# Kernel tuning notes

Measured on AMD Instinct MI355X. Metric: run time of the kernel, lower is better.

## Reference

```python
import jax, jax.numpy as jnp
import numpy as np

B, S, DIM = 2, 2048, 2048
NUM_HEADS, HEAD_DIM, KV_PER = 16, 128, 1
NUM_KV = NUM_HEADS * KV_PER  # = 16; code requires KV_PER == 1 for shape consistency
QKV_OUT = (NUM_HEADS + 2 * NUM_KV) * HEAD_DIM


def setup_inputs() -> dict:
    key = jax.random.key(0)
    k1, k2, k3 = jax.random.split(key, 3)
    x = jax.random.normal(k1, (B, S, DIM), dtype=jnp.float32)
    w_qkv = jax.random.normal(k2, (DIM, QKV_OUT), dtype=jnp.float32) * (DIM ** -0.5)
    w_out = jax.random.normal(k3, (NUM_HEADS * HEAD_DIM, DIM), dtype=jnp.float32) * ((NUM_HEADS * HEAD_DIM) ** -0.5)
    return {"x": x, "w_qkv": w_qkv, "w_out": w_out}


def reference(x, w_qkv, w_out):
    b, s, _ = x.shape
    # QKV projection, then split heads: [b, s, nq + 2*nkv, d]
    qkv = (x @ w_qkv).reshape(b, s, NUM_HEADS + 2 * NUM_KV, HEAD_DIM)
    q = qkv[:, :, :NUM_HEADS]                          # [b, s, nq, d]
    k = qkv[:, :, NUM_HEADS:NUM_HEADS + NUM_KV]        # [b, s, nkv, d]
    v = qkv[:, :, NUM_HEADS + NUM_KV:]                 # [b, s, nkv, d]
    # query -> [b, nkv, per, s, d] (per == KV_PER == 1)
    q = q.reshape(b, s, NUM_KV, KV_PER, HEAD_DIM).transpose(0, 2, 3, 1, 4)
    k = k.transpose(0, 2, 1, 3)                        # [b, nkv, s, d]
    v = v.transpose(0, 2, 1, 3)                        # [b, nkv, s, d]
    scale = 1.0 / (HEAD_DIM ** 0.5)
    # logits: [b, nkv, per, s_q, s_k]
    logits = jnp.einsum('bkpsd,bktd->bkpst', q, k) * scale
    attn = jax.nn.softmax(logits.astype(jnp.float32), axis=-1)
    # combined: [b, nkv, per, s, d] -> [b, s, nkv, per, d] -> [b, s, dim]
    combined = jnp.einsum('bkpst,bktd->bkpsd', attn, v.astype(jnp.float32)).astype(v.dtype)
    combined = combined.transpose(0, 3, 1, 2, 4).reshape(b, s, NUM_KV * KV_PER * HEAD_DIM)
    return combined @ w_out
```

## Files before the change

kernel.cpp:

```cpp
#include <hip/hip_runtime.h>
#include <cstdint>

typedef __bf16 bf16x8 __attribute__((ext_vector_type(8)));
typedef float f32x4 __attribute__((ext_vector_type(4)));
typedef unsigned short u16x8 __attribute__((ext_vector_type(8)));

#define NH 16
#define HD 128
#define SEQ 2048
#define DIM 2048
#define QKVO 6144

__device__ __forceinline__ unsigned short f32_bf16(float f) {
  uint32_t u = __builtin_bit_cast(uint32_t, f);
  u += 0x7fffu + ((u >> 16) & 1u);
  return (unsigned short)(u >> 16);
}

__device__ __forceinline__ uint32_t cvt_pk_bf16(float a, float b) {
  uint32_t r;
  asm("v_cvt_pk_bf16_f32 %0, %1, %2" : "=v"(r) : "v"(a), "v"(b));
  return r;
}

__device__ __forceinline__ void gl2lds16(const void* g, void* l) {
  __builtin_amdgcn_global_load_lds(
      (const __attribute__((address_space(1))) uint32_t*)g,
      (__attribute__((address_space(3))) uint32_t*)l,
      16, 0, 0);
}

__global__ __launch_bounds__(256) void cvt_f32_bf16(
    const float* __restrict__ in, unsigned short* __restrict__ out) {
  long i = ((long)blockIdx.x * 256 + threadIdx.x) * 8;
  f32x4 a = *(const f32x4*)(in + i);
  f32x4 b = *(const f32x4*)(in + i + 4);
  u16x8 r;
#pragma unroll
  for (int j = 0; j < 4; j++) { r[j] = f32_bf16(a[j]); r[4 + j] = f32_bf16(b[j]); }
  *(u16x8*)(out + i) = r;
}

__global__ __launch_bounds__(256) void transpose_f32_bf16(
    const float* __restrict__ in, unsigned short* __restrict__ out,
    int R, int C) {
  __shared__ unsigned short tile[64][65];
  const int t = threadIdx.x, tx = t & 63, ty = t >> 6;
  const long r0 = (long)blockIdx.y * 64, c0 = (long)blockIdx.x * 64;
  for (int i = 0; i < 16; i++) {
    int row = ty + i * 4;
    tile[row][tx] = f32_bf16(in[(r0 + row) * C + c0 + tx]);
  }
  __syncthreads();
  for (int i = 0; i < 16; i++) {
    int row = ty + i * 4;
    out[(c0 + row) * R + r0 + tx] = tile[tx][row];
  }
}

__global__ __launch_bounds__(256) void transpose_v(
    const unsigned short* __restrict__ qkv, unsigned short* __restrict__ vT) {
  __shared__ unsigned short tile[64][65];
  const int t = threadIdx.x, tx = t & 63, ty = t >> 6;
  const int bh = blockIdx.z, b = bh >> 4, h = bh & 15;
  const long t0 = (long)blockIdx.x * 64;
  const int d0 = blockIdx.y * 64;
  const unsigned short* src = qkv + (long)b * SEQ * QKVO + 2 * NH * HD + h * HD;
  for (int i = 0; i < 16; i++) {
    int row = ty + i * 4;
    tile[row][tx] = src[(t0 + row) * QKVO + d0 + tx];
  }
  __syncthreads();
  unsigned short* dst = vT + ((long)bh * HD + d0) * SEQ + t0;
  for (int i = 0; i < 16; i++) {
    int row = ty + i * 4;
    dst[(long)row * SEQ + tx] = tile[tx][row];
  }
}

template <typename OutT>
__global__ __launch_bounds__(256) void gemm_bt(
    const unsigned short* __restrict__ A, int lda,
    const unsigned short* __restrict__ BT, int ldb,
    OutT* __restrict__ C, int ldc, int K) {
  __shared__ __align__(16) unsigned short As[128 * 32];
  __shared__ __align__(16) unsigned short Bs[128 * 32];
  const int t = threadIdx.x;
  const int lane = t & 63, w = t >> 6;
  const int quad = lane >> 4, l16 = lane & 15;
  const int wm = (w & 1) * 64, wn = (w >> 1) * 64;
  const long m0 = (long)blockIdx.y * 128, n0 = (long)blockIdx.x * 128;

  f32x4 acc[4][4] = {};
  const int rowA = t >> 2, kslot = (t & 3) * 8;
  const unsigned short* Ag = A + (m0 + rowA) * (long)lda + kslot;
  const unsigned short* Bg = BT + (n0 + rowA) * (long)ldb + kslot;
  unsigned short* AsBase = &As[w * 512];
  unsigned short* BsBase = &Bs[w * 512];

  for (int k0 = 0; k0 < K; k0 += 32) {
    __syncthreads();
    gl2lds16(Ag + k0, AsBase);
    gl2lds16(Ag + 64 * (long)lda + k0, AsBase + 2048);
    gl2lds16(Bg + k0, BsBase);
    gl2lds16(Bg + 64 * (long)ldb + k0, BsBase + 2048);
    __syncthreads();

    bf16x8 af[4], bf[4];
#pragma unroll
    for (int mt = 0; mt < 4; mt++)
      af[mt] = *(const bf16x8*)&As[(wm + mt * 16 + l16) * 32 + quad * 8];
#pragma unroll
    for (int nt = 0; nt < 4; nt++)
      bf[nt] = *(const bf16x8*)&Bs[(wn + nt * 16 + l16) * 32 + quad * 8];
#pragma unroll
    for (int mt = 0; mt < 4; mt++)
#pragma unroll
      for (int nt = 0; nt < 4; nt++)
        acc[mt][nt] = __builtin_amdgcn_mfma_f32_16x16x32_bf16(
            af[mt], bf[nt], acc[mt][nt], 0, 0, 0);
  }

#pragma unroll
  for (int mt = 0; mt < 4; mt++) {
    long row = m0 + wm + mt * 16 + quad * 4;
#pragma unroll
    for (int r = 0; r < 4; r++) {
      OutT* crow = C + (row + r) * (long)ldc + n0 + wn + l16;
#pragma unroll
      for (int nt = 0; nt < 4; nt++) {
        float v = acc[mt][nt][r];
        if constexpr (sizeof(OutT) == 2) crow[nt * 16] = f32_bf16(v);
        else                             crow[nt * 16] = v;
      }
    }
  }
}

#define KSTR 136
#define VSTR 72
__global__ __launch_bounds__(256, 2) void attn_kernel(
    unsigned short* qkv, const unsigned short* __restrict__ vT) {
  __shared__ __align__(16) unsigned short Ks[64 * KSTR];
  __shared__ __align__(16) unsigned short Vs[128 * VSTR];
  __shared__ __align__(16) unsigned short Ps[4][32 * VSTR];

  const int t = threadIdx.x, lane = t & 63, w = t >> 6;
  const int quad = lane >> 4, l16 = lane & 15;
  const int q0 = blockIdx.x * 128, h = blockIdx.y, b = blockIdx.z;
  const long row0 = (long)b * SEQ;

  bf16x8 qf[2][4];
#pragma unroll
  for (int mt = 0; mt < 2; mt++) {
    const unsigned short* Qp =
        qkv + (row0 + q0 + w * 32 + mt * 16 + l16) * (long)QKVO + h * HD + quad * 8;
#pragma unroll
    for (int c = 0; c < 4; c++) qf[mt][c] = *(const bf16x8*)(Qp + c * 32);
  }

  float m_l[2], l_l[2];
  f32x4 o[2][8] = {};
  m_l[0] = m_l[1] = -1e30f;
  l_l[0] = l_l[1] = 0.f;
  const float c2 = 0.08838834764831845f * 1.4426950408889634f;
  const float thr = 8.0f / c2;

  const unsigned short* Kg = qkv + row0 * QKVO + NH * HD + h * HD;
  const unsigned short* Vg = vT + ((long)(b * NH + h)) * HD * SEQ;

  bf16x8 kr[4], vr[4];
#pragma unroll
  for (int i = 0; i < 4; i++) {
    int s = i * 256 + t;
    kr[i] = *(const bf16x8*)(Kg + (long)(s >> 4) * QKVO + (s & 15) * 8);
  }
#pragma unroll
  for (int i = 0; i < 4; i++) {
    int s = i * 256 + t;
    vr[i] = *(const bf16x8*)(Vg + (long)(s >> 3) * SEQ + (s & 7) * 8);
  }

  for (int kc = 0; kc < SEQ; kc += 64) {
    __syncthreads();
#pragma unroll
    for (int i = 0; i < 4; i++) {
      int s = i * 256 + t;
      *(bf16x8*)&Ks[(s >> 4) * KSTR + (s & 15) * 8] = kr[i];
    }
#pragma unroll
    for (int i = 0; i < 4; i++) {
      int s = i * 256 + t;
      *(bf16x8*)&Vs[(s >> 3) * VSTR + (s & 7) * 8] = vr[i];
    }
    __syncthreads();

    if (kc + 64 < SEQ) {
#pragma unroll
      for (int i = 0; i < 4; i++) {
        int s = i * 256 + t;
        kr[i] = *(const bf16x8*)(Kg + (long)(kc + 64 + (s >> 4)) * QKVO + (s & 15) * 8);
      }
#pragma unroll
      for (int i = 0; i < 4; i++) {
        int s = i * 256 + t;
        vr[i] = *(const bf16x8*)(Vg + (long)(s >> 3) * SEQ + kc + 64 + (s & 7) * 8);
      }
    }

    f32x4 st[2][4];
#pragma unroll
    for (int kt = 0; kt < 4; kt++) {
      f32x4 a0 = {}, a1 = {};
#pragma unroll
      for (int c = 0; c < 4; c++) {
        bf16x8 kf = *(const bf16x8*)&Ks[(kt * 16 + l16) * KSTR + c * 32 + quad * 8];
        a0 = __builtin_amdgcn_mfma_f32_16x16x32_bf16(kf, qf[0][c], a0, 0, 0, 0);
        a1 = __builtin_amdgcn_mfma_f32_16x16x32_bf16(kf, qf[1][c], a1, 0, 0, 0);
      }
      st[0][kt] = a0; st[1][kt] = a1;
    }

#pragma unroll
    for (int mt = 0; mt < 2; mt++) {
      float mx0 = fmaxf(fmaxf(st[mt][0][0], st[mt][0][1]),
                        fmaxf(st[mt][0][2], st[mt][0][3]));
      float mx1 = fmaxf(fmaxf(st[mt][1][0], st[mt][1][1]),
                        fmaxf(st[mt][1][2], st[mt][1][3]));
      float mx2 = fmaxf(fmaxf(st[mt][2][0], st[mt][2][1]),
                        fmaxf(st[mt][2][2], st[mt][2][3]));
      float mx3 = fmaxf(fmaxf(st[mt][3][0], st[mt][3][1]),
                        fmaxf(st[mt][3][2], st[mt][3][3]));
      float mx = fmaxf(fmaxf(mx0, mx1), fmaxf(mx2, mx3));
      mx = fmaxf(mx, __shfl_xor(mx, 16, 64));
      mx = fmaxf(mx, __shfl_xor(mx, 32, 64));

      if (__any(mx > m_l[mt] + thr)) {
        float mn = fmaxf(m_l[mt], mx);
        float alpha = exp2f(c2 * (m_l[mt] - mn));
        m_l[mt] = mn;
        l_l[mt] *= alpha;
        float a_o[4];
#pragma unroll
        for (int r = 0; r < 4; r++) a_o[r] = __shfl(alpha, (quad << 2) | r, 16);
#pragma unroll
        for (int dt = 0; dt < 8; dt++)
#pragma unroll
          for (int r = 0; r < 4; r++) o[mt][dt][r] *= a_o[r];
      }

      float cm = c2 * m_l[mt];
      float sum = 0.f;
      uint32_t pk0[4], pk1[4];
#pragma unroll
      for (int kt = 0; kt < 4; kt++) {
        float p0 = exp2f(fmaf(st[mt][kt][0], c2, -cm));
        float p1 = exp2f(fmaf(st[mt][kt][1], c2, -cm));
        float p2 = exp2f(fmaf(st[mt][kt][2], c2, -cm));
        float p3 = exp2f(fmaf(st[mt][kt][3], c2, -cm));
        sum += (p0 + p1) + (p2 + p3);
        pk0[kt] = cvt_pk_bf16(p0, p1);
        pk1[kt] = cvt_pk_bf16(p2, p3);
      }
      sum += __shfl_xor(sum, 16, 64);
      sum += __shfl_xor(sum, 32, 64);
      l_l[mt] += sum;

#pragma unroll
      for (int kt = 0; kt < 4; kt++) {
        uint2 w2; w2.x = pk0[kt]; w2.y = pk1[kt];
        *(uint2*)&Ps[w][(mt * 16 + l16) * VSTR + kt * 16 + quad * 4] = w2;
      }
    }
    asm volatile("s_waitcnt lgkmcnt(0)" ::: "memory");

#pragma unroll
    for (int cc = 0; cc < 2; cc++) {
      bf16x8 pf0 = *(const bf16x8*)&Ps[w][(l16) * VSTR + cc * 32 + quad * 8];
      bf16x8 pf1 = *(const bf16x8*)&Ps[w][(16 + l16) * VSTR + cc * 32 + quad * 8];
#pragma unroll
      for (int dt = 0; dt < 8; dt++) {
        bf16x8 vf = *(const bf16x8*)&Vs[(dt * 16 + l16) * VSTR + cc * 32 + quad * 8];
        o[0][dt] = __builtin_amdgcn_mfma_f32_16x16x32_bf16(pf0, vf, o[0][dt], 0, 0, 0);
        o[1][dt] = __builtin_amdgcn_mfma_f32_16x16x32_bf16(pf1, vf, o[1][dt], 0, 0, 0);
      }
    }
  }

  float inv_o[2][4];
#pragma unroll
  for (int mt = 0; mt < 2; mt++) {
    float linv = 1.f / l_l[mt];
#pragma unroll
    for (int r = 0; r < 4; r++) inv_o[mt][r] = __shfl(linv, (quad << 2) | r, 16);
  }
#pragma unroll
  for (int mt = 0; mt < 2; mt++) {
    long orow = row0 + q0 + w * 32 + mt * 16 + quad * 4;
    unsigned short* Op = qkv + orow * (long)QKVO + h * HD + l16;
#pragma unroll
    for (int r = 0; r < 4; r++) {
#pragma unroll
      for (int dt = 0; dt < 8; dt++)
        Op[(long)r * QKVO + dt * 16] = f32_bf16(o[mt][dt][r] * inv_o[mt][r]);
    }
  }
}

extern "C" void kernel_launch(void* const* d_in, const int* in_sizes, int n_in,
                              void* d_out, int out_size, void* d_ws, size_t ws_size,
                              hipStream_t stream) {
  const float* x     = (const float*)d_in[0];
  const float* w_qkv = (const float*)d_in[1];
  const float* w_out = (const float*)d_in[2];
  float* out = (float*)d_out;

  char* ws = (char*)d_ws;
  unsigned short* qkv   = (unsigned short*)ws;
  unsigned short* xbf   = (unsigned short*)(ws + 50331648);
  unsigned short* wqkvT = (unsigned short*)(ws + 67108864);
  unsigned short* vTbuf = (unsigned short*)(ws + 67108864);
  unsigned short* woutT = (unsigned short*)(ws + 83886080);

  dim3 blk(256);
  cvt_f32_bf16<<<4096, blk, 0, stream>>>(x, xbf);
  transpose_f32_bf16<<<dim3(QKVO / 64, DIM / 64), blk, 0, stream>>>(w_qkv, wqkvT, DIM, QKVO);
  gemm_bt<unsigned short><<<dim3(QKVO / 128, 4096 / 128), blk, 0, stream>>>(
      xbf, DIM, wqkvT, DIM, qkv, QKVO, DIM);
  transpose_v<<<dim3(SEQ / 64, HD / 64, 2 * NH), blk, 0, stream>>>(qkv, vTbuf);
  transpose_f32_bf16<<<dim3(DIM / 64, DIM / 64), blk, 0, stream>>>(w_out, woutT, DIM, DIM);
  attn_kernel<<<dim3(SEQ / 128, NH, 2), blk, 0, stream>>>(qkv, vTbuf);
  gemm_bt<float><<<dim3(DIM / 128, 4096 / 128), blk, 0, stream>>>(
      qkv, QKVO, woutT, DIM, out, DIM, DIM);
}
```

Measured before the change: 430.6 us.

## Use 256x256 tiled 8-wave GEMM with staged async loads for QKV projection

Adds a new bf16 GEMM kernel using 256x256 output tiles, 512 threads and a double-buffered LDS pipeline. Global-to-LDS copies for the next K tile are interleaved with MFMA quadrants, separated by barriers and priority hints. It replaces the 128x128 GEMM for the QKV projection to raise data reuse per tile and hide load latency. The grid shrinks to 24x16 = 384 blocks, so wave balance across CUs changes and the barrier count per iteration goes up.

```diff
diff --git a/kernel.cpp b/kernel.cpp
--- a/kernel.cpp
+++ b/kernel.cpp
@@ -137,6 +137,126 @@
   }
 }
 
+template <typename OutT>
+__global__ __launch_bounds__(512, 2) void gemm256_bt(
+    const unsigned short* __restrict__ A, int lda,
+    const unsigned short* __restrict__ BT, int ldb,
+    OutT* __restrict__ C, int ldc, int K) {
+  __shared__ __align__(16) unsigned short As[2][16384];
+  __shared__ __align__(16) unsigned short Bs[2][16384];
+  const int t = threadIdx.x, lane = t & 63, w = t >> 6;
+  const int l16 = lane & 15, quad = lane >> 4;
+  const int wn = w & 3, wm = w >> 2;
+  const long m0 = (long)blockIdx.y * 256, n0 = (long)blockIdx.x * 256;
+  const int NT = K >> 6;
+
+  const int srow = (w << 3) + (lane >> 3);
+  const int sgr = (lane & 7) ^ (lane >> 3);
+  const unsigned short* Ag = A + (m0 + srow) * (long)lda + sgr * 8;
+  const unsigned short* Bg = BT + (n0 + srow) * (long)ldb + sgr * 8;
+
+  const int g0 = ((quad ^ (l16 & 7)) << 3);
+  const int aBase = wm * 8192 + l16 * 64;
+  const int bBase = (wn >> 1) * 8192 + (((wn & 1) << 6) + l16) * 64;
+
+  f32x4 acc[8][4] = {};
+  bf16x8 af[4][2], bfr[2][2];
+
+  auto stageA = [&](int half, int buf, long k0) {
+    const unsigned short* src = Ag + (long)half * 128 * lda + k0;
+    unsigned short* dst = &As[buf][half * 8192 + (w << 3) * 64];
+    gl2lds16(src, dst);
+    gl2lds16(src + 64 * (long)lda, dst + 4096);
+  };
+  auto stageB = [&](int half, int buf, long k0) {
+    const unsigned short* src = Bg + (long)half * 128 * ldb + k0;
+    unsigned short* dst = &Bs[buf][half * 8192 + (w << 3) * 64];
+    gl2lds16(src, dst);
+    gl2lds16(src + 64 * (long)ldb, dst + 4096);
+  };
+  auto readA = [&](int buf, int mh) {
+#pragma unroll
+    for (int mf = 0; mf < 4; ++mf)
+#pragma unroll
+      for (int ks = 0; ks < 2; ++ks)
+        af[mf][ks] = *(const bf16x8*)
+            &As[buf][aBase + (mh * 64 + mf * 16) * 64 + (g0 ^ (ks << 5))];
+  };
+  auto readB = [&](int buf, int nh) {
+#pragma unroll
+    for (int nf = 0; nf < 2; ++nf)
+#pragma unroll
+      for (int ks = 0; ks < 2; ++ks)
+        bfr[nf][ks] = *(const bf16x8*)
+            &Bs[buf][bBase + (nh * 32 + nf * 16) * 64 + (g0 ^ (ks << 5))];
+  };
+  auto quad16 = [&](int mh, int nh) {
+#pragma unroll
+    for (int mf = 0; mf < 4; ++mf)
+#pragma unroll
+      for (int nf = 0; nf < 2; ++nf)
+#pragma unroll
+        for (int ks = 0; ks < 2; ++ks)
+          acc[mh * 4 + mf][nh * 2 + nf] = __builtin_amdgcn_mfma_f32_16x16x32_bf16(
+              af[mf][ks], bfr[nf][ks], acc[mh * 4 + mf][nh * 2 + nf], 0, 0, 0);
+  };
+
+#define GBAR asm volatile("s_barrier" ::: "memory")
+
+  stageA(0, 0, 0); stageA(1, 0, 0); stageB(0, 0, 0); stageB(1, 0, 0);
+  if (NT > 1) { stageA(0, 1, 64); asm volatile("s_waitcnt vmcnt(2)" ::: "memory"); }
+  else        { asm volatile("s_waitcnt vmcnt(0)" ::: "memory"); }
+  GBAR;
+
+  for (int T = 0; T < NT; ++T) {
+    const int bufc = T & 1, bufn = bufc ^ 1;
+    const long k0n = ((long)T + 1) << 6, k0nn = ((long)T + 2) << 6;
+    const bool sN1 = (T + 1 < NT), sN2 = (T + 2 < NT);
+    readA(bufc, 0); readB(bufc, 0);
+    if (sN1) stageA(1, bufn, k0n);
+    GBAR;
+    __builtin_amdgcn_s_setprio(1); quad16(0, 0); __builtin_amdgcn_s_setprio(0);
+    GBAR;
+    readB(bufc, 1);
+    if (sN1) stageB(0, bufn, k0n);
+    GBAR;
+    __builtin_amdgcn_s_setprio(1); quad16(0, 1); __builtin_amdgcn_s_setprio(0);
+    GBAR;
+    readA(bufc, 1);
+    if (sN1) stageB(1, bufn, k0n);
+    GBAR;
+    __builtin_amdgcn_s_setprio(1); quad16(1, 1); __builtin_amdgcn_s_setprio(0);
+    GBAR;
+    readB(bufc, 0);
+    if (sN2) stageA(0, bufc, k0nn);
+    GBAR;
+    __builtin_amdgcn_s_setprio(1); quad16(1, 0); __builtin_amdgcn_s_setprio(0);
+    if (sN2)      asm volatile("s_waitcnt vmcnt(2)" ::: "memory");
+    else if (sN1) asm volatile("s_waitcnt vmcnt(0)" ::: "memory");
+    GBAR;
+  }
+
+#pragma unroll
+  for (int mh = 0; mh < 2; ++mh)
+#pragma unroll
+    for (int mf = 0; mf < 4; ++mf) {
+      const long row = m0 + wm * 128 + mh * 64 + mf * 16 + quad * 4;
+#pragma unroll
+      for (int r = 0; r < 4; ++r) {
+        OutT* crow = C + (row + r) * (long)ldc + n0 + wn * 64 + l16;
+#pragma unroll
+        for (int nh = 0; nh < 2; ++nh)
+#pragma unroll
+          for (int nf = 0; nf < 2; ++nf) {
+            float v = acc[mh * 4 + mf][nh * 2 + nf][r];
+            if constexpr (sizeof(OutT) == 2) crow[nh * 32 + nf * 16] = f32_bf16(v);
+            else                             crow[nh * 32 + nf * 16] = v;
+          }
+      }
+    }
+#undef GBAR
+}
+
 #define KSTR 136
 #define VSTR 72
 __global__ __launch_bounds__(256, 2) void attn_kernel(
@@ -325,7 +445,7 @@
   dim3 blk(256);
   cvt_f32_bf16<<<4096, blk, 0, stream>>>(x, xbf);
   transpose_f32_bf16<<<dim3(QKVO / 64, DIM / 64), blk, 0, stream>>>(w_qkv, wqkvT, DIM, QKVO);
-  gemm_bt<unsigned short><<<dim3(QKVO / 128, 4096 / 128), blk, 0, stream>>>(
+  gemm256_bt<unsigned short><<<dim3(QKVO / 256, 4096 / 256), dim3(512), 0, stream>>>(
       xbf, DIM, wqkvT, DIM, qkv, QKVO, DIM);
   transpose_v<<<dim3(SEQ / 64, HD / 64, 2 * NH), blk, 0, stream>>>(qkv, vTbuf);
   transpose_f32_bf16<<<dim3(DIM / 64, DIM / 64), blk, 0, stream>>>(w_out, woutT, DIM, DIM);
```

Result: no change. 422.6 us (-1.9%).

## Use 256x256-tile triple-buffered GEMM for QKV projection

Applied to the files above, without the earlier changes.

Adds a new bf16 MFMA GEMM kernel with 256x256 block tiles, 512 threads, and a three-stage LDS ring filled by direct global-to-LDS loads with XOR-swizzled layout. It replaces the 128x128 GEMM for the QKV projection only, aiming for more data reuse per block and for overlapping loads with MFMA work. The cost is higher register pressure (128 accumulator floats per thread), 96KB of LDS, and only 384 blocks, which may limit occupancy and tail balance.

```diff
diff --git a/kernel.cpp b/kernel.cpp
--- a/kernel.cpp
+++ b/kernel.cpp
@@ -137,6 +137,87 @@
   }
 }
 
+template <typename OutT>
+__global__ __launch_bounds__(512, 2) void gemm256_bt(
+    const unsigned short* __restrict__ A, int lda,
+    const unsigned short* __restrict__ BT, int ldb,
+    OutT* __restrict__ C, int ldc, int K) {
+  __shared__ __align__(16) unsigned short As[3][8192];
+  __shared__ __align__(16) unsigned short Bs[3][8192];
+  const int t = threadIdx.x, lane = t & 63, w = t >> 6;
+  const int l16 = lane & 15, quad = lane >> 4;
+  const int wn = w & 3, wm = w >> 2;
+  const int NT = K >> 5;
+  const long m0 = (long)blockIdx.y * 256, n0 = (long)blockIdx.x * 256;
+
+  const int srow = t >> 2;
+  const int sgr = (t & 3) ^ ((srow >> 1) & 3);
+  const unsigned short* Ag = A + (m0 + srow) * (long)lda + sgr * 8;
+  const unsigned short* Bg = BT + (n0 + srow) * (long)ldb + sgr * 8;
+
+  const int pg = quad ^ ((l16 >> 1) & 3);
+  const int aBase = (wm * 128 + l16) * 32 + pg * 8;
+  const int bBase = (wn * 64 + l16) * 32 + pg * 8;
+
+  f32x4 acc[8][4] = {};
+
+  auto stage = [&](int buf, long k0) {
+    gl2lds16(Ag + k0, &As[buf][w * 512]);
+    gl2lds16(Ag + 128 * (long)lda + k0, &As[buf][4096 + w * 512]);
+    gl2lds16(Bg + k0, &Bs[buf][w * 512]);
+    gl2lds16(Bg + 128 * (long)ldb + k0, &Bs[buf][4096 + w * 512]);
+  };
+
+#define GBAR asm volatile("s_barrier" ::: "memory")
+
+  stage(0, 0);
+  if (NT > 1) stage(1, 32);
+  asm volatile("s_waitcnt vmcnt(0)" ::: "memory");
+  GBAR;
+
+  int c = 0;
+  for (int T = 0; T < NT; ++T) {
+    const bool s2 = (T + 2 < NT), s1 = (T + 1 < NT);
+    const int s = (c == 0) ? 2 : c - 1;
+    if (s2) stage(s, ((long)T + 2) << 5);
+
+    bf16x8 bf[4], af[8];
+#pragma unroll
+    for (int nf = 0; nf < 4; ++nf)
+      bf[nf] = *(const bf16x8*)&Bs[c][bBase + nf * 512];
+#pragma unroll
+    for (int mf = 0; mf < 8; ++mf)
+      af[mf] = *(const bf16x8*)&As[c][aBase + mf * 512];
+#pragma unroll
+    for (int mf = 0; mf < 8; ++mf)
+#pragma unroll
+      for (int nf = 0; nf < 4; ++nf)
+        acc[mf][nf] = __builtin_amdgcn_mfma_f32_16x16x32_bf16(
+            af[mf], bf[nf], acc[mf][nf], 0, 0, 0);
+
+    if (s2)      asm volatile("s_waitcnt vmcnt(4)" ::: "memory");
+    else if (s1) asm volatile("s_waitcnt vmcnt(0)" ::: "memory");
+    GBAR;
+    c = (c == 2) ? 0 : c + 1;
+  }
+
+#pragma unroll
+  for (int mf = 0; mf < 8; ++mf) {
+    const long row = m0 + wm * 128 + mf * 16 + quad * 4;
+#pragma unroll
+    for (int r = 0; r < 4; ++r) {
+      OutT* crow = C + (row + r) * (long)ldc + n0 + wn * 64 + l16;
+#pragma unroll
+      for (int nf = 0; nf < 4; ++nf) {
+        float v = acc[mf][nf][r];
+        if constexpr (sizeof(OutT) == 2) crow[nf * 16] = f32_bf16(v);
+        else                             crow[nf * 16] = v;
+      }
+    }
+  }
+#undef GBAR
+}
+
 #define KSTR 136
 #define VSTR 72
 __global__ __launch_bounds__(256, 2) void attn_kernel(
@@ -325,7 +406,7 @@
   dim3 blk(256);
   cvt_f32_bf16<<<4096, blk, 0, stream>>>(x, xbf);
   transpose_f32_bf16<<<dim3(QKVO / 64, DIM / 64), blk, 0, stream>>>(w_qkv, wqkvT, DIM, QKVO);
-  gemm_bt<unsigned short><<<dim3(QKVO / 128, 4096 / 128), blk, 0, stream>>>(
+  gemm256_bt<unsigned short><<<dim3(QKVO / 256, 4096 / 256), dim3(512), 0, stream>>>(
       xbf, DIM, wqkvT, DIM, qkv, QKVO, DIM);
   transpose_v<<<dim3(SEQ / 64, HD / 64, 2 * NH), blk, 0, stream>>>(qkv, vTbuf);
   transpose_f32_bf16<<<dim3(DIM / 64, DIM / 64), blk, 0, stream>>>(w_out, woutT, DIM, DIM);
```

New measurement: 460.9 us. 7.0% more time.
